# Optimization experiments

Hardware: AMD Instinct MI355X
Metric: run time of the kernel (lower is better)

Reference implementation:

```python
import jax, jax.numpy as jnp
import numpy as np

B, Q_LEN, K_LEN = 2, 2048, 2048
Q_CH, K_CH = 1024, 1024
H, D = 16, 64  # head_num, head_dim = q_channels // head_num
TEMPERATURE = (H * D) ** 0.5  # use_tube=False -> sqrt(1024)=32


def setup_inputs() -> dict:
    key = jax.random.key(0)
    ks = jax.random.split(key, 14)
    s = 0.02
    return {
        "q": jax.random.normal(ks[0], (B, Q_LEN, Q_CH), jnp.float32),
        "k": jax.random.normal(ks[1], (B, K_LEN, K_CH), jnp.float32),
        "v": jax.random.normal(ks[2], (B, K_LEN, K_CH), jnp.float32),
        "mask": jax.random.randint(ks[3], (B, Q_LEN, K_LEN), 0, 2) == 1,
        "attn_bias": jax.random.normal(ks[4], (B, H, Q_LEN, K_LEN), jnp.float32),
        # weights stored [in, out] (math-equivalent to torch Linear's x @ W.T + b)
        "Wq": jax.random.normal(ks[5], (Q_CH, H * D), jnp.float32) * s,
        "bq": jnp.zeros((H * D,), jnp.float32),
        "Wk": jax.random.normal(ks[6], (K_CH, H * D), jnp.float32) * s,
        "bk": jnp.zeros((H * D,), jnp.float32),
        "Wv": jax.random.normal(ks[7], (K_CH, H * D), jnp.float32) * s,
        "bv": jnp.zeros((H * D,), jnp.float32),
        "Wo": jax.random.normal(ks[8], (H * D, Q_CH), jnp.float32) * s,
        "bo": jnp.zeros((Q_CH,), jnp.float32),
    }


def reference(q, k, v, mask, attn_bias, Wq, bq, Wk, bk, Wv, bv, Wo, bo):
    b, q_len = q.shape[0], q.shape[1]
    k_len = k.shape[1]
    # projections + head split: [b, len, H, D] -> [b, H, len, D]
    qh = (q @ Wq + bq).reshape(b, q_len, H, D).transpose(0, 2, 1, 3)
    kh = (k @ Wk + bk).reshape(b, k_len, H, D).transpose(0, 2, 1, 3)
    vh = (v @ Wv + bv).reshape(b, k_len, H, D).transpose(0, 2, 1, 3)
    # scores [b, H, q_len, k_len]
    scores = jnp.einsum("bhqd,bhkd->bhqk", qh, kh) / TEMPERATURE + attn_bias
    scores = jnp.where(mask[:, None, :, :], -jnp.inf, scores)
    attn = jax.nn.softmax(scores, axis=-1)
    # dropout is identity in eval / deterministic reference
    out = jnp.einsum("bhqk,bhkd->bhqd", attn, vh)
    out = out.transpose(0, 2, 1, 3).reshape(b, q_len, H * D)
    out = out @ Wo + bo
    return out, attn
```

## Files before the change

### kernel.cpp

```cpp
#include <hip/hip_runtime.h>
#include <hip/hip_bf16.h>


typedef __attribute__((ext_vector_type(8))) short bf16x8;
typedef __attribute__((ext_vector_type(8))) _Float16 f16x8;
typedef __attribute__((ext_vector_type(4))) float f32x4;
typedef __attribute__((ext_vector_type(4))) int i32x4;
typedef __attribute__((ext_vector_type(4))) _Float16 f16x4;
typedef unsigned short u16;

#define NB 2
#define QL 2048
#define KL 2048
#define CH 1024
#define NH 16
#define HD 64
#define SH_STRIDE 2600

__device__ __forceinline__ u16 f2bf(float f){
  unsigned u = __float_as_uint(f);
  u += 0x7fffu + ((u >> 16) & 1u);
  return (u16)(u >> 16);
}
__device__ __forceinline__ u16 f2h(float f){
  _Float16 h = (_Float16)f;
  return *(u16*)&h;
}

__global__ void k_detect(const unsigned int* __restrict__ m, int* __restrict__ flag){
  unsigned v = m[threadIdx.x];
  unsigned long long b = __ballot(v > 1u);
  __shared__ int r[4];
  if ((threadIdx.x & 63) == 0) r[threadIdx.x >> 6] = (b != 0ULL);
  __syncthreads();
  if (threadIdx.x == 0) *flag = (r[0] | r[1] | r[2] | r[3]);
}

__global__ __launch_bounds__(256) void k_maskpack(const void* __restrict__ maskp, const int* __restrict__ flag,
                                                  unsigned* __restrict__ mbits){
  const int idx = blockIdx.x*256 + threadIdx.x;
  unsigned out = 0;
  if (*flag){
    const unsigned* m8 = (const unsigned*)maskp + (size_t)idx*8;
    #pragma unroll
    for (int j=0;j<8;++j){
      unsigned wv = m8[j];
      out |= ((wv & 1u) | ((wv>>7)&2u) | ((wv>>14)&4u) | ((wv>>21)&8u)) << (4*j);
    }
  } else {
    const i32x4* m32 = (const i32x4*)maskp + (size_t)idx*8;
    #pragma unroll
    for (int j=0;j<8;++j){
      i32x4 v = m32[j];
      out |= (unsigned)((v[0]&1) | ((v[1]&1)<<1) | ((v[2]&1)<<2) | ((v[3]&1)<<3)) << (4*j);
    }
  }
  mbits[idx] = out;
}

__global__ __launch_bounds__(256) void k_cvt(const float* __restrict__ q, const float* __restrict__ k,
                                             const float* __restrict__ v,
                                             u16* __restrict__ qc, u16* __restrict__ kc, u16* __restrict__ vc){
  const float* in = blockIdx.y==0 ? q : blockIdx.y==1 ? k : v;
  u16* out = blockIdx.y==0 ? qc : blockIdx.y==1 ? kc : vc;
  const size_t i = ((size_t)blockIdx.x*256 + threadIdx.x)*8;
  float4 lo = *(const float4*)&in[i];
  float4 hi = *(const float4*)&in[i+4];
  ushort4 a, b;
  a.x=f2bf(lo.x); a.y=f2bf(lo.y); a.z=f2bf(lo.z); a.w=f2bf(lo.w);
  b.x=f2bf(hi.x); b.y=f2bf(hi.y); b.z=f2bf(hi.z); b.w=f2bf(hi.w);
  *(ushort4*)&out[i] = a;
  *(ushort4*)&out[i+4] = b;
}

__global__ __launch_bounds__(256) void k_transpose(const float* __restrict__ Wq, const float* __restrict__ Wk,
                                                   const float* __restrict__ Wv, const float* __restrict__ Wo,
                                                   u16* __restrict__ wt){
  const float* src = blockIdx.z==0 ? Wq : blockIdx.z==1 ? Wk : blockIdx.z==2 ? Wv : Wo;
  u16* dst = wt + (size_t)blockIdx.z * CH * CH;
  __shared__ float t[32][33];
  const int x = blockIdx.x*32, y = blockIdx.y*32;
  const int tx = threadIdx.x & 31, ty = threadIdx.x >> 5;
  #pragma unroll
  for (int j=0;j<32;j+=8) t[ty+j][tx] = src[(size_t)(y+ty+j)*CH + x + tx];
  __syncthreads();
  #pragma unroll
  for (int j=0;j<32;j+=8) dst[(size_t)(x+ty+j)*CH + y + tx] = f2bf(t[tx][ty+j]);
}

__device__ __forceinline__ void gemm128_core(const u16* __restrict__ A, const u16* __restrict__ Bt,
                                             int m0, int n0, f32x4 acc[2][4]){
  __shared__ u16 As[128*64];
  __shared__ u16 Bs[128*64];
  const int tid = threadIdx.x, lane = tid & 63, w = tid >> 6;
  const int wm = w >> 1, wn = w & 1;
  const int lr = lane & 15, lg = lane >> 4;
  for (int k0 = 0; k0 < CH; k0 += 64){
    #pragma unroll
    for (int r=0;r<2;++r){
      const int chunk = r*512 + tid;
      const int row = chunk >> 3, ch = chunk & 7;
      __builtin_amdgcn_global_load_lds(
        (const __attribute__((address_space(1))) void*)&A[(size_t)(m0+row)*CH + k0 + ch*8],
        (__attribute__((address_space(3))) void*)&As[(r*512 + w*64)*8], 16, 0, 0);
      __builtin_amdgcn_global_load_lds(
        (const __attribute__((address_space(1))) void*)&Bt[(size_t)(n0+row)*CH + k0 + ch*8],
        (__attribute__((address_space(3))) void*)&Bs[(r*512 + w*64)*8], 16, 0, 0);
    }
    __syncthreads();
    #pragma unroll
    for (int kk=0; kk<2; ++kk){
      bf16x8 a0 = *(const bf16x8*)&As[(wm*32      + lr)*64 + (kk*4+lg)*8];
      bf16x8 a1 = *(const bf16x8*)&As[(wm*32 + 16 + lr)*64 + (kk*4+lg)*8];
      #pragma unroll
      for (int fj=0;fj<4;++fj){
        bf16x8 b = *(const bf16x8*)&Bs[(wn*64 + fj*16 + lr)*64 + (kk*4+lg)*8];
        acc[0][fj] = __builtin_amdgcn_mfma_f32_16x16x32_bf16(a0, b, acc[0][fj], 0,0,0);
        acc[1][fj] = __builtin_amdgcn_mfma_f32_16x16x32_bf16(a1, b, acc[1][fj], 0,0,0);
      }
    }
    __syncthreads();
  }
}

__global__ __launch_bounds__(512) void k_gemm_qkv3(const u16* __restrict__ qc, const u16* __restrict__ kc,
                                                   const u16* __restrict__ vc, const u16* __restrict__ wt,
                                                   const float* __restrict__ bq, const float* __restrict__ bk,
                                                   const float* __restrict__ bv,
                                                   u16* __restrict__ qh, u16* __restrict__ kh, u16* __restrict__ vt){
  const int z = blockIdx.x >> 3;
  const int n0 = (blockIdx.x & 7) * 128;
  const int m0 = blockIdx.y * 128;
  const u16* A  = z==0 ? qc : z==1 ? kc : vc;
  const u16* Bt = wt + (size_t)z*CH*CH;
  const float* bias = z==0 ? bq : z==1 ? bk : bv;
  const float scale = z==0 ? 0.03125f : 1.0f;
  u16* qk_dst = z==0 ? qh : kh;
  f32x4 acc[2][4] = {};
  gemm128_core(A, Bt, m0, n0, acc);
  const int lane = threadIdx.x & 63, w = threadIdx.x >> 6;
  const int wm = w >> 1, wn = w & 1;
  const int lr = lane & 15, lg = lane >> 4;
  #pragma unroll
  for (int fi=0;fi<2;++fi)
  #pragma unroll
  for (int fj=0;fj<4;++fj)
  #pragma unroll
  for (int r=0;r<4;++r){
    int row = m0 + wm*32 + fi*16 + lg*4 + r;
    int col = n0 + wn*64 + fj*16 + lr;
    float val = (acc[fi][fj][r] + bias[col]) * scale;
    int bb = row >> 11, ll = row & 2047, hh = col >> 6, dd = col & 63;
    if (z < 2) qk_dst[(((size_t)(bb*NH+hh)*QL + ll) << 6) + dd] = f2bf(val);
    else       vt[(((size_t)(bb*NH+hh) << 6) + dd)*KL + ll] = f2h(val);
  }
}

__global__ __launch_bounds__(512) void k_gemm_out3(const u16* __restrict__ ao, const u16* __restrict__ wto,
                                                   const float* __restrict__ bo, float* __restrict__ out){
  const int n0 = blockIdx.x * 128, m0 = blockIdx.y * 128;
  f32x4 acc[2][4] = {};
  gemm128_core(ao, wto, m0, n0, acc);
  const int lane = threadIdx.x & 63, w = threadIdx.x >> 6;
  const int wm = w >> 1, wn = w & 1;
  const int lr = lane & 15, lg = lane >> 4;
  #pragma unroll
  for (int fi=0;fi<2;++fi)
  #pragma unroll
  for (int fj=0;fj<4;++fj)
  #pragma unroll
  for (int r=0;r<4;++r){
    int row = m0 + wm*32 + fi*16 + lg*4 + r;
    int col = n0 + wn*64 + fj*16 + lr;
    out[(size_t)row*CH + col] = acc[fi][fj][r] + bo[col];
  }
}

__global__ __launch_bounds__(256) void k_gemm_qkv(const float* __restrict__ q, const float* __restrict__ k,
                                                  const float* __restrict__ v, const u16* __restrict__ wt,
                                                  const float* __restrict__ bq, const float* __restrict__ bk,
                                                  const float* __restrict__ bv,
                                                  u16* __restrict__ qh, u16* __restrict__ kh, u16* __restrict__ vt){
  const int z = blockIdx.z;
  const float* A = z==0 ? q : z==1 ? k : v;
  const u16* Bt = wt + (size_t)z*CH*CH;
  const float* bias = z==0 ? bq : z==1 ? bk : bv;
  u16* Cp = z==0 ? qh : z==1 ? kh : vt;
  const float scale = (z==0) ? 0.03125f : 1.0f;
  __shared__ u16 As[64][72];
  __shared__ u16 Bs[64][72];
  const int m0 = blockIdx.y*64, n0 = blockIdx.x*64;
  const int tid = threadIdx.x, lane = tid & 63, w = tid >> 6;
  const int wm = w >> 1, wn = w & 1;
  const int lr = lane & 15, lg = lane >> 4;
  f32x4 acc[2][2] = {};
  for (int k0 = 0; k0 < CH; k0 += 64){
    #pragma unroll
    for (int j=0;j<4;++j){
      int idx = tid + 256*j, r = idx >> 4, c = (idx & 15)*4;
      float4 vv = *(const float4*)&A[(size_t)(m0+r)*CH + k0 + c];
      ushort4 s; s.x=f2bf(vv.x); s.y=f2bf(vv.y); s.z=f2bf(vv.z); s.w=f2bf(vv.w);
      *(ushort4*)&As[r][c] = s;
    }
    #pragma unroll
    for (int j=0;j<2;++j){
      int idx = tid + 256*j, r = idx >> 3, c = (idx & 7)*8;
      *(uint4*)&Bs[r][c] = *(const uint4*)&Bt[(size_t)(n0+r)*CH + k0 + c];
    }
    __syncthreads();
    #pragma unroll
    for (int kk=0; kk<2; ++kk){
      bf16x8 a0 = *(const bf16x8*)&As[wm*32      + lr][kk*32 + lg*8];
      bf16x8 a1 = *(const bf16x8*)&As[wm*32 + 16 + lr][kk*32 + lg*8];
      bf16x8 b0 = *(const bf16x8*)&Bs[wn*32      + lr][kk*32 + lg*8];
      bf16x8 b1 = *(const bf16x8*)&Bs[wn*32 + 16 + lr][kk*32 + lg*8];
      acc[0][0] = __builtin_amdgcn_mfma_f32_16x16x32_bf16(a0,b0,acc[0][0],0,0,0);
      acc[0][1] = __builtin_amdgcn_mfma_f32_16x16x32_bf16(a0,b1,acc[0][1],0,0,0);
      acc[1][0] = __builtin_amdgcn_mfma_f32_16x16x32_bf16(a1,b0,acc[1][0],0,0,0);
      acc[1][1] = __builtin_amdgcn_mfma_f32_16x16x32_bf16(a1,b1,acc[1][1],0,0,0);
    }
    __syncthreads();
  }
  #pragma unroll
  for (int fi=0;fi<2;++fi)
  #pragma unroll
  for (int fj=0;fj<2;++fj)
  #pragma unroll
  for (int r=0;r<4;++r){
    int row = m0 + wm*32 + fi*16 + lg*4 + r;
    int col = n0 + wn*32 + fj*16 + lr;
    float val = (acc[fi][fj][r] + bias[col]) * scale;
    int bb = row >> 11, ll = row & 2047, hh = col >> 6, dd = col & 63;
    if (z < 2) Cp[(((size_t)(bb*NH+hh)*QL + ll) << 6) + dd] = f2bf(val);
    else       Cp[(((size_t)(bb*NH+hh) << 6) + dd)*KL + ll] = f2h(val);
  }
}

__global__ __launch_bounds__(256) void k_gemm_out(const u16* __restrict__ Ap, const u16* __restrict__ Bt,
                                                  const float* __restrict__ bias, float* __restrict__ Cp){
  __shared__ u16 As[64][72];
  __shared__ u16 Bs[64][72];
  const int m0 = blockIdx.y*64, n0 = blockIdx.x*64;
  const int tid = threadIdx.x, lane = tid & 63, w = tid >> 6;
  const int wm = w >> 1, wn = w & 1;
  const int lr = lane & 15, lg = lane >> 4;
  f32x4 acc[2][2] = {};
  for (int k0 = 0; k0 < CH; k0 += 64){
    #pragma unroll
    for (int j=0;j<2;++j){
      int idx = tid + 256*j, r = idx >> 3, c = (idx & 7)*8;
      *(uint4*)&As[r][c] = *(const uint4*)&Ap[(size_t)(m0+r)*CH + k0 + c];
      *(uint4*)&Bs[r][c] = *(const uint4*)&Bt[(size_t)(n0+r)*CH + k0 + c];
    }
    __syncthreads();
    #pragma unroll
    for (int kk=0; kk<2; ++kk){
      bf16x8 a0 = *(const bf16x8*)&As[wm*32      + lr][kk*32 + lg*8];
      bf16x8 a1 = *(const bf16x8*)&As[wm*32 + 16 + lr][kk*32 + lg*8];
      bf16x8 b0 = *(const bf16x8*)&Bs[wn*32      + lr][kk*32 + lg*8];
      bf16x8 b1 = *(const bf16x8*)&Bs[wn*32 + 16 + lr][kk*32 + lg*8];
      acc[0][0] = __builtin_amdgcn_mfma_f32_16x16x32_bf16(a0,b0,acc[0][0],0,0,0);
      acc[0][1] = __builtin_amdgcn_mfma_f32_16x16x32_bf16(a0,b1,acc[0][1],0,0,0);
      acc[1][0] = __builtin_amdgcn_mfma_f32_16x16x32_bf16(a1,b0,acc[1][0],0,0,0);
      acc[1][1] = __builtin_amdgcn_mfma_f32_16x16x32_bf16(a1,b1,acc[1][1],0,0,0);
    }
    __syncthreads();
  }
  #pragma unroll
  for (int fi=0;fi<2;++fi)
  #pragma unroll
  for (int fj=0;fj<2;++fj)
  #pragma unroll
  for (int r=0;r<4;++r){
    int row = m0 + wm*32 + fi*16 + lg*4 + r;
    int col = n0 + wn*32 + fj*16 + lr;
    Cp[(size_t)row*CH + col] = acc[fi][fj][r] + bias[col];
  }
}

template<int BITS>
__global__ __launch_bounds__(1024, 1) void k_attn(const u16* __restrict__ qh, const u16* __restrict__ kh,
                                              const _Float16* __restrict__ vt, const float* __restrict__ bias,
                                              const void* __restrict__ maskp, const int* __restrict__ flag,
                                              const unsigned* __restrict__ mbits,
                                              float* __restrict__ attn, u16* __restrict__ ao){
  __shared__ _Float16 Sh[16][SH_STRIDE];
  __shared__ float osum[8][16][17];
  __shared__ float wsum[16][16];
  __shared__ float inv_l[16];
  const int qt = BITS ? blockIdx.x : blockIdx.y;
  const int h  = BITS ? blockIdx.y : blockIdx.x;
  const int b  = blockIdx.z;
  const int q0 = qt*16, bh = b*NH + h;
  const int tid = threadIdx.x, lane = tid & 63, w = tid >> 6;
  const int lr = lane & 15, lg = lane >> 4;
  const u16* qb = qh + ((size_t)bh*QL + q0)*HD;
  const bf16x8 qf0 = *(const bf16x8*)&qb[lr*HD +      lg*8];
  const bf16x8 qf1 = *(const bf16x8*)&qb[lr*HD + 32 + lg*8];
  const float* bb = bias + ((size_t)bh*QL + q0)*KL;
  const u16* khb = kh + (size_t)bh*KL*HD;
  const _Float16* vtb = vt + (size_t)bh*HD*KL;
  const int c0 = w*128;

  f32x4 bi[8];
  unsigned mwd[8];
  #pragma unroll
  for (int ct=0; ct<8; ++ct){
    const int cb = c0 + ct*16 + lg*4;
    bi[ct] = *(const f32x4*)&bb[(size_t)lr*KL + cb];
    if (BITS) mwd[ct] = mbits[((size_t)b*QL + q0 + lr)*(KL/32) + (cb>>5)];
  }
  const int isbool = BITS ? 0 : *flag;
  const unsigned char* mb8 = (const unsigned char*)maskp + ((size_t)b*QL + q0)*KL;
  const int* mb32 = (const int*)maskp + ((size_t)b*QL + q0)*KL;

  float ps = 0.f;
  #pragma unroll
  for (int ct=0; ct<8; ++ct){
    const int cb = c0 + ct*16 + lg*4;
    f32x4 acc = bi[ct];
    const int kcol = c0 + ct*16 + lr;
    bf16x8 kf0 = *(const bf16x8*)&khb[(size_t)kcol*HD +      lg*8];
    bf16x8 kf1 = *(const bf16x8*)&khb[(size_t)kcol*HD + 32 + lg*8];
    acc = __builtin_amdgcn_mfma_f32_16x16x32_bf16(kf0, qf0, acc, 0,0,0);
    acc = __builtin_amdgcn_mfma_f32_16x16x32_bf16(kf1, qf1, acc, 0,0,0);
    unsigned msel;
    i32x4 mv;
    if (BITS){
      msel = (mwd[ct] >> (cb & 31)) & 0xFu;
    } else if (isbool){
      unsigned mw = *(const unsigned*)&mb8[(size_t)lr*KL + cb];
      msel = (mw&1u) | ((mw>>7)&2u) | ((mw>>14)&4u) | ((mw>>21)&8u);
    } else {
      mv = *(const i32x4*)&mb32[(size_t)lr*KL + cb];
      msel = (unsigned)((mv[0]&1) | ((mv[1]&1)<<1) | ((mv[2]&1)<<2) | ((mv[3]&1)<<3));
    }
    f16x4 sv;
    #pragma unroll
    for (int r=0;r<4;++r){
      float e = ((msel >> r) & 1u) ? 0.f : __expf(acc[r]);
      sv[r] = (_Float16)e;
      ps += e;
    }
    *(f16x4*)&Sh[lr][cb] = sv;
  }
  ps += __shfl_xor(ps, 16);
  ps += __shfl_xor(ps, 32);
  if (lane < 16) wsum[w][lr] = ps;
  __syncthreads();
  if (tid < 16){
    float s = 0.f;
    #pragma unroll
    for (int ww=0; ww<16; ++ww) s += wsum[ww][tid];
    inv_l[tid] = 1.f / s;
  }
  __syncthreads();

  if (w < 8){
    const int d0 = (w & 3)*16, kb0 = (w >> 2)*1024;
    f32x4 oacc = {};
    #pragma unroll
    for (int kb=0; kb<4; ++kb){
      f16x8 vf[8];
      #pragma unroll
      for (int i=0;i<8;++i)
        vf[i] = *(const f16x8*)&vtb[(size_t)(d0+lr)*KL + kb0 + kb*256 + i*32 + lg*8];
      #pragma unroll
      for (int i=0;i<8;++i){
        f16x8 a = *(const f16x8*)&Sh[lr][kb0 + kb*256 + i*32 + lg*8];
        oacc = __builtin_amdgcn_mfma_f32_16x16x32_f16(a, vf[i], oacc, 0,0,0);
      }
    }
    #pragma unroll
    for (int r=0;r<4;++r) osum[w][lg*4+r][lr] = oacc[r];
  } else {
    float* ob = attn + ((size_t)bh*QL + q0)*KL;
    const int r0 = (w - 8)*2;
    #pragma unroll
    for (int rr=0; rr<2; ++rr){
      const int row = r0 + rr;
      const float ivr = inv_l[row];
      #pragma unroll
      for (int ch=0; ch<8; ++ch){
        f16x4 hv = *(const f16x4*)&Sh[row][ch*256 + lane*4];
        f32x4 v;
        v[0]=(float)hv[0]*ivr; v[1]=(float)hv[1]*ivr; v[2]=(float)hv[2]*ivr; v[3]=(float)hv[3]*ivr;
        *(f32x4*)&ob[(size_t)row*KL + ch*256 + lane*4] = v;
      }
    }
  }
  __syncthreads();
  {
    const int row = tid >> 6, d = tid & 63;
    float o = (osum[d >> 4][row][d & 15] + osum[4 + (d >> 4)][row][d & 15]) * inv_l[row];
    ao[((size_t)b*QL + q0 + row)*CH + h*HD + d] = f2bf(o);
  }
}

extern "C" void kernel_launch(void* const* d_in, const int* in_sizes, int n_in,
                              void* d_out, int out_size, void* d_ws, size_t ws_size,
                              hipStream_t stream){
  const float* q    = (const float*)d_in[0];
  const float* k    = (const float*)d_in[1];
  const float* v    = (const float*)d_in[2];
  const void*  mask = d_in[3];
  const float* bias = (const float*)d_in[4];
  const float* Wq   = (const float*)d_in[5];
  const float* bq   = (const float*)d_in[6];
  const float* Wk   = (const float*)d_in[7];
  const float* bk   = (const float*)d_in[8];
  const float* Wv   = (const float*)d_in[9];
  const float* bv   = (const float*)d_in[10];
  const float* Wo   = (const float*)d_in[11];
  const float* bo   = (const float*)d_in[12];

  char* wsb = (char*)d_ws;
  int* flag = (int*)wsb;
  u16* qh = (u16*)(wsb + 256);
  u16* kh = (u16*)(wsb + 256 + 1*8388608);
  u16* vt = (u16*)(wsb + 256 + 2*8388608);
  u16* ao = (u16*)(wsb + 256 + 3*8388608);
  u16* wt = (u16*)(wsb + 256 + 4*8388608);
  unsigned* mbits = (unsigned*)(wsb + 256 + 5*8388608);
  u16* qc = (u16*)(wsb + 256 + 5*8388608 + 1048576);
  u16* kc = qc + (size_t)NB*QL*CH;
  u16* vc = kc + (size_t)NB*QL*CH;
  const size_t need_bits = 256 + 5ull*8388608 + 1048576;
  const size_t need_conv = need_bits + 3ull*NB*QL*CH*2;
  const bool usebits = (ws_size >= need_bits);
  const bool useconv = (ws_size >= need_conv);

  float* out  = (float*)d_out;
  float* attn = out + (size_t)NB*QL*CH;

  k_detect<<<1, 256, 0, stream>>>((const unsigned int*)mask, flag);
  if (usebits)
    k_maskpack<<<dim3(1024), 256, 0, stream>>>(mask, flag, mbits);
  k_transpose<<<dim3(32,32,4), 256, 0, stream>>>(Wq, Wk, Wv, Wo, wt);
  if (useconv){
    k_cvt<<<dim3(2048,3), 256, 0, stream>>>(q, k, v, qc, kc, vc);
    k_gemm_qkv3<<<dim3(24,32), 512, 0, stream>>>(qc, kc, vc, wt, bq, bk, bv, qh, kh, vt);
  } else {
    k_gemm_qkv<<<dim3(16,64,3), 256, 0, stream>>>(q, k, v, wt, bq, bk, bv, qh, kh, vt);
  }
  if (usebits)
    k_attn<1><<<dim3(128,16,2), 1024, 0, stream>>>(qh, kh, (const _Float16*)vt, bias, mask, flag, mbits, attn, ao);
  else
    k_attn<0><<<dim3(16,128,2), 1024, 0, stream>>>(qh, kh, (const _Float16*)vt, bias, mask, flag, mbits, attn, ao);
  if (useconv)
    k_gemm_out3<<<dim3(8,32), 512, 0, stream>>>(ao, wt + 3145728, bo, out);
  else
    k_gemm_out<<<dim3(16,64), 256, 0, stream>>>(ao, wt + 3145728, bo, out);
}
```

Measured before the change: 554.8 us.

## Add 32-row query tile attention kernel to halve K/V reloads per block

Replaces the 16-query-row attention kernel with a new kernel that handles 32 query rows per block, using two 16-row groups that share the same K and V streams. Score exponentials are staged in a larger fp16 shared buffer. Half the waves do the PV matmul while the other half write normalized attention probabilities out. This is meant to cut repeated K/V global reads and halve the number of blocks, at the cost of more shared memory and possibly lower occupancy.

```diff
diff --git a/kernel.cpp b/kernel.cpp
--- a/kernel.cpp
+++ b/kernel.cpp
@@ -16,6 +16,7 @@
 #define NH 16
 #define HD 64
 #define SH_STRIDE 2600
+#define S32_STRIDE 2344
 
 __device__ __forceinline__ u16 f2bf(float f){
   unsigned u = __float_as_uint(f);
@@ -275,6 +276,108 @@
     int row = m0 + wm*32 + fi*16 + lg*4 + r;
     int col = n0 + wn*32 + fj*16 + lr;
     Cp[(size_t)row*CH + col] = acc[fi][fj][r] + bias[col];
+  }
+}
+
+__global__ __launch_bounds__(1024, 1) void k_attn32(const u16* __restrict__ qh, const u16* __restrict__ kh,
+                                              const _Float16* __restrict__ vt, const float* __restrict__ bias,
+                                              const unsigned* __restrict__ mbits,
+                                              float* __restrict__ attn, u16* __restrict__ ao){
+  __shared__ _Float16 Sh[32][S32_STRIDE];
+  __shared__ float wsum[16][32];
+  __shared__ float inv_l[32];
+  const int qt = blockIdx.x, h = blockIdx.y, b = blockIdx.z;
+  const int q0 = qt*32, bh = b*NH + h;
+  const int tid = threadIdx.x, lane = tid & 63, w = tid >> 6;
+  const int lr = lane & 15, lg = lane >> 4;
+  const float* bb = bias + ((size_t)bh*QL + q0)*KL;
+  const u16* khb = kh + (size_t)bh*KL*HD;
+  const _Float16* vtb = vt + (size_t)bh*HD*KL;
+  const int c0 = w*128;
+
+  #pragma unroll
+  for (int g=0; g<2; ++g){
+    const int qrow = q0 + g*16;
+    const u16* qb = qh + ((size_t)bh*QL + qrow)*HD;
+    const bf16x8 qf0 = *(const bf16x8*)&qb[lr*HD +      lg*8];
+    const bf16x8 qf1 = *(const bf16x8*)&qb[lr*HD + 32 + lg*8];
+    f32x4 bi[8];
+    unsigned mwd[8];
+    #pragma unroll
+    for (int ct=0; ct<8; ++ct){
+      const int cb = c0 + ct*16 + lg*4;
+      bi[ct] = *(const f32x4*)&bb[(size_t)(g*16+lr)*KL + cb];
+      mwd[ct] = mbits[((size_t)b*QL + qrow + lr)*(KL/32) + (cb>>5)];
+    }
+    float ps = 0.f;
+    #pragma unroll
+    for (int ct=0; ct<8; ++ct){
+      const int cb = c0 + ct*16 + lg*4;
+      f32x4 acc = bi[ct];
+      const int kcol = c0 + ct*16 + lr;
+      bf16x8 kf0 = *(const bf16x8*)&khb[(size_t)kcol*HD +      lg*8];
+      bf16x8 kf1 = *(const bf16x8*)&khb[(size_t)kcol*HD + 32 + lg*8];
+      acc = __builtin_amdgcn_mfma_f32_16x16x32_bf16(kf0, qf0, acc, 0,0,0);
+      acc = __builtin_amdgcn_mfma_f32_16x16x32_bf16(kf1, qf1, acc, 0,0,0);
+      const unsigned msel = (mwd[ct] >> (cb & 31)) & 0xFu;
+      f16x4 sv;
+      #pragma unroll
+      for (int r=0;r<4;++r){
+        float e = ((msel >> r) & 1u) ? 0.f : __expf(acc[r]);
+        sv[r] = (_Float16)e;
+        ps += e;
+      }
+      *(f16x4*)&Sh[g*16+lr][cb] = sv;
+    }
+    ps += __shfl_xor(ps, 16);
+    ps += __shfl_xor(ps, 32);
+    if (lane < 16) wsum[w][g*16+lr] = ps;
+  }
+  __syncthreads();
+  if (tid < 32){
+    float s = 0.f;
+    #pragma unroll
+    for (int ww=0; ww<16; ++ww) s += wsum[ww][tid];
+    inv_l[tid] = 1.f / s;
+  }
+  __syncthreads();
+
+  if (w < 8){
+    const int d0 = (w & 3)*16, rh = (w >> 2)*16;
+    f32x4 oacc = {};
+    #pragma unroll
+    for (int kb=0; kb<8; ++kb){
+      f16x8 vf[8], af[8];
+      #pragma unroll
+      for (int i=0;i<8;++i){
+        vf[i] = *(const f16x8*)&vtb[(size_t)(d0+lr)*KL + kb*256 + i*32 + lg*8];
+        af[i] = *(const f16x8*)&Sh[rh+lr][kb*256 + i*32 + lg*8];
+      }
+      #pragma unroll
+      for (int i=0;i<8;++i)
+        oacc = __builtin_amdgcn_mfma_f32_16x16x32_f16(af[i], vf[i], oacc, 0,0,0);
+    }
+    #pragma unroll
+    for (int r=0;r<4;++r){
+      const int row = rh + lg*4 + r;
+      ao[((size_t)b*QL + q0 + row)*CH + h*HD + d0 + lr] = f2bf(oacc[r] * inv_l[row]);
+    }
+  } else {
+    float* ob = attn + ((size_t)bh*QL + q0)*KL;
+    const int r0 = (w - 8)*4;
+    #pragma unroll
+    for (int rr=0; rr<4; ++rr){
+      const int row = r0 + rr;
+      const float ivr = inv_l[row];
+      float* orow = ob + (size_t)row*KL;
+      #pragma unroll
+      for (int ch=0; ch<8; ++ch){
+        f16x4 hv = *(const f16x4*)&Sh[row][ch*256 + lane*4];
+        f32x4 v;
+        v[0]=(float)hv[0]*ivr; v[1]=(float)hv[1]*ivr; v[2]=(float)hv[2]*ivr; v[3]=(float)hv[3]*ivr;
+        *(f32x4*)&orow[ch*256 + lane*4] = v;
+      }
+    }
   }
 }
 
@@ -444,7 +547,7 @@
     k_gemm_qkv<<<dim3(16,64,3), 256, 0, stream>>>(q, k, v, wt, bq, bk, bv, qh, kh, vt);
   }
   if (usebits)
-    k_attn<1><<<dim3(128,16,2), 1024, 0, stream>>>(qh, kh, (const _Float16*)vt, bias, mask, flag, mbits, attn, ao);
+    k_attn32<<<dim3(64,16,2), 1024, 0, stream>>>(qh, kh, (const _Float16*)vt, bias, mbits, attn, ao);
   else
     k_attn<0><<<dim3(16,128,2), 1024, 0, stream>>>(qh, kh, (const _Float16*)vt, bias, mask, flag, mbits, attn, ao);
   if (useconv)
```

New measurement: 540.0 us. -2.7%, faster.
